# Kernel tuning notes

Measured on AMD Instinct MI355X. Metric: run time of the kernel, lower is better.

Reference implementation:

```python
import jax, jax.numpy as jnp
import numpy as np

N_NODES = 50000


def _gcn_conv(x, row, col, W, b, n_nodes):
    """PyG GCNConv: symmetric-normalized scatter-add aggregation.
    row/col already include self-loops. x: [N, Fin], W: [Fin, Fout]."""
    h = x @ W  # [N, Fout]
    deg = jax.ops.segment_sum(jnp.ones(col.shape[0], x.dtype), col,
                              num_segments=n_nodes)  # in-degree incl. self-loops
    dis = jnp.where(deg > 0, jax.lax.rsqrt(deg), 0.0)  # deg^{-1/2}
    norm = dis[row] * dis[col]  # [E+N]
    msg = h[row] * norm[:, None]  # gather + scale, [E+N, Fout]
    out = jax.ops.segment_sum(msg, col, num_segments=n_nodes)  # scatter-add
    return out + b


def setup_inputs() -> dict:
    key = jax.random.key(0)
    k1, k2, k3, k4 = jax.random.split(key, 4)
    N, E, FIN, FH = N_NODES, 800000, 512, 512
    x = jax.random.normal(k1, (N, FIN), dtype=jnp.float32)
    edge_index = jax.random.randint(k2, (2, E), 0, N, dtype=jnp.int64)
    W1 = jax.random.normal(k3, (FIN, FH), dtype=jnp.float32) * (1.0 / np.sqrt(FIN))
    b1 = jnp.zeros((FH,), jnp.float32)
    W2 = jax.random.normal(k4, (FH, FH), dtype=jnp.float32) * (1.0 / np.sqrt(FH))
    b2 = jnp.zeros((FH,), jnp.float32)
    return {"x": x, "edge_index": edge_index, "W1": W1, "b1": b1,
            "W2": W2, "b2": b2}


def reference(x, edge_index, W1, b1, W2, b2):
    n = x.shape[0]
    loops = jnp.arange(n, dtype=edge_index.dtype)
    row = jnp.concatenate([edge_index[0], loops])  # sources
    col = jnp.concatenate([edge_index[1], loops])  # targets
    h = _gcn_conv(x, row, col, W1, b1, n)
    h = jax.nn.relu(h)
    return _gcn_conv(h, row, col, W2, b2, n)
```

## Files before the change

kernel.cpp:

```cpp
#include <hip/hip_runtime.h>
#include <hip/hip_bf16.h>

typedef short short8 __attribute__((ext_vector_type(8)));
typedef unsigned short u16x8 __attribute__((ext_vector_type(8)));
typedef float f32x4 __attribute__((ext_vector_type(4)));

#define AS1 __attribute__((address_space(1)))
#define AS3 __attribute__((address_space(3)))

__device__ __forceinline__ void gload16(const void* g, void* l) {
  __builtin_amdgcn_global_load_lds((AS1 void*)g, (AS3 void*)l, 16, 0, 0);
}

__device__ __forceinline__ unsigned short f2bf(float f) {
  unsigned u = __float_as_uint(f);
  u = (u + 0x7FFF + ((u >> 16) & 1)) >> 16;
  return (unsigned short)u;
}
__device__ __forceinline__ float bf2f(unsigned short u) {
  return __uint_as_float(((unsigned)u) << 16);
}

__global__ void prep_kernel(const float4* __restrict__ x4, ushort4* __restrict__ xb4, int n4,
                            const float* __restrict__ W1, unsigned short* __restrict__ W1t,
                            const float* __restrict__ W2, unsigned short* __restrict__ W2t) {
  const int nthr = gridDim.x * 256;
  for (int i = blockIdx.x * 256 + threadIdx.x; i < n4; i += nthr) {
    float4 v = x4[i];
    ushort4 o;
    o.x = f2bf(v.x); o.y = f2bf(v.y); o.z = f2bf(v.z); o.w = f2bf(v.w);
    xb4[i] = o;
  }
  for (int idx = blockIdx.x * 256 + threadIdx.x; idx < 512 * 512; idx += nthr) {
    const int k = idx >> 9, n = idx & 511;
    W1t[n * 512 + k] = f2bf(W1[idx]);
    W2t[n * 512 + k] = f2bf(W2[idx]);
  }
}

__global__ void detect64_kernel(const int* __restrict__ ei32, int* __restrict__ flag) {
  if (blockIdx.x == 0 && threadIdx.x == 0) {
    int f = 1;
    for (int i = 0; i < 64; ++i)
      if (ei32[2 * i + 1] != 0) { f = 0; break; }
    *flag = f;
  }
}

__global__ void count_kernel(const int* __restrict__ ei32, const int* __restrict__ flag,
                             int* __restrict__ cnt, int E) {
  int e = blockIdx.x * 256 + threadIdx.x;
  if (e >= E) return;
  int c = (*flag) ? ei32[2 * E + 2 * e] : ei32[E + e];
  atomicAdd(&cnt[c], 1);
}

__global__ void __launch_bounds__(1024) scan_bsum_kernel(const int* __restrict__ cnt,
                                                         int* __restrict__ bsum, int n) {
  __shared__ int ws[16];
  const int tid = threadIdx.x, lane = tid & 63, wid = tid >> 6;
  const int i = blockIdx.x * 1024 + tid;
  int x = (i < n) ? cnt[i] : 0;
#pragma unroll
  for (int d = 1; d < 64; d <<= 1) x += __shfl_xor(x, d, 64);
  if (lane == 0) ws[wid] = x;
  __syncthreads();
  if (tid == 0) {
    int s = 0;
#pragma unroll
    for (int w = 0; w < 16; ++w) s += ws[w];
    bsum[blockIdx.x] = s;
  }
}

__global__ void scan_boff_kernel(int* __restrict__ bsum, int* __restrict__ total, int B) {
  const int lane = threadIdx.x;
  const int v = (lane < B) ? bsum[lane] : 0;
  int x = v;
#pragma unroll
  for (int d = 1; d < 64; d <<= 1) {
    int y = __shfl_up(x, d, 64);
    if (lane >= d) x += y;
  }
  if (lane < B) bsum[lane] = x - v;
  if (lane == B - 1) *total = x;
}

__global__ void __launch_bounds__(1024) scan_fill_kernel(const int* __restrict__ cnt,
    const int* __restrict__ boff, int* __restrict__ ptr, int* __restrict__ cur,
    float* __restrict__ dis, int n) {
  __shared__ int ws[16];
  const int tid = threadIdx.x, lane = tid & 63, wid = tid >> 6;
  const int i = blockIdx.x * 1024 + tid;
  const int v = (i < n) ? cnt[i] : 0;
  int x = v;
#pragma unroll
  for (int d = 1; d < 64; d <<= 1) {
    int y = __shfl_up(x, d, 64);
    if (lane >= d) x += y;
  }
  if (lane == 63) ws[wid] = x;
  __syncthreads();
  if (tid < 16) {
    int wv = ws[tid];
    int wx = wv;
#pragma unroll
    for (int d = 1; d < 16; d <<= 1) {
      int y = __shfl_up(wx, d, 64);
      if (tid >= d) wx += y;
    }
    ws[tid] = wx - wv;
  }
  __syncthreads();
  if (i < n) {
    const int excl = boff[blockIdx.x] + ws[wid] + (x - v);
    ptr[i] = excl;
    cur[i] = excl;
    dis[i] = rsqrtf((float)(v + 1));
  }
}

__global__ void fill_kernel(const int* __restrict__ ei32, const int* __restrict__ flag,
                            int* __restrict__ cur, int* __restrict__ eidx, int E) {
  int e = blockIdx.x * 256 + threadIdx.x;
  if (e >= E) return;
  int is64 = *flag;
  int r = is64 ? ei32[2 * e] : ei32[e];
  int c = is64 ? ei32[2 * E + 2 * e] : ei32[E + e];
  int pos = atomicAdd(&cur[c], 1);
  eidx[pos] = r;
}

__global__ void __launch_bounds__(256) gemm_kernel(const unsigned short* __restrict__ A,
                                                   const unsigned short* __restrict__ Bt,
                                                   const float* __restrict__ dscale,
                                                   unsigned short* __restrict__ C, int M) {
  __shared__ alignas(128) unsigned short As[2][8192];
  __shared__ alignas(128) unsigned short Bs[2][8192];
  const int tid = threadIdx.x;
  const int wave = tid >> 6, lane = tid & 63;
  const int wm = wave >> 1, wn = wave & 1;

  const int nbm = (M + 127) >> 7;
  const int nwg = nbm * 4;
  const int orig = blockIdx.x;
  const int xcd = orig & 7;
  const int q8 = nwg >> 3, r8 = nwg & 7;
  const int wg = (xcd < r8 ? xcd * (q8 + 1) : r8 * (q8 + 1) + (xcd - r8) * q8) + (orig >> 3);
  const int bn = wg & 3;
  const int bm = wg >> 2;

  const int lr = lane >> 3, ls = lane & 7;
  const int fr = lane & 15, ks = lane >> 4;

  f32x4 acc[4][4] = {};

#define STAGE(BUF, KO)                                                                     \
  {                                                                                        \
    _Pragma("unroll") for (int i = 0; i < 4; ++i) {                                        \
      int ra = bm * 128 + i * 32 + wave * 8 + lr;                                          \
      ra = ra < M ? ra : M - 1;                                                            \
      gload16(A + (size_t)ra * 512 + (KO) + ((ls ^ (lr & 7)) << 3),                        \
              &As[BUF][(i * 32 + wave * 8) * 64]);                                         \
      const int rb = bn * 128 + i * 32 + wave * 8 + lr;                                    \
      gload16(Bt + (size_t)rb * 512 + (KO) + ((ls ^ (lr & 7)) << 3),                       \
              &Bs[BUF][(i * 32 + wave * 8) * 64]);                                         \
    }                                                                                      \
  }

  STAGE(0, 0)
  __syncthreads();

  int buf = 0;
  for (int kt = 0; kt < 8; ++kt) {
    if (kt < 7) STAGE(buf ^ 1, (kt + 1) * 64)

    short8 af[2][4], bfg[2][4];
#pragma unroll
    for (int m = 0; m < 4; ++m) {
      const int tr = wm * 64 + m * 16 + fr;
      af[0][m] = *(const short8*)&As[buf][tr * 64 + (((ks * 8)      ) ^ ((tr & 7) << 3))];
      af[1][m] = *(const short8*)&As[buf][tr * 64 + (((ks * 8) + 32 ) ^ ((tr & 7) << 3))];
    }
#pragma unroll
    for (int n = 0; n < 4; ++n) {
      const int tb = wn * 64 + n * 16 + fr;
      bfg[0][n] = *(const short8*)&Bs[buf][tb * 64 + (((ks * 8)      ) ^ ((tb & 7) << 3))];
      bfg[1][n] = *(const short8*)&Bs[buf][tb * 64 + (((ks * 8) + 32 ) ^ ((tb & 7) << 3))];
    }
#pragma unroll
    for (int kk = 0; kk < 2; ++kk)
#pragma unroll
      for (int m = 0; m < 4; ++m)
#pragma unroll
        for (int n = 0; n < 4; ++n)
          acc[m][n] = __builtin_amdgcn_mfma_f32_16x16x32_bf16(af[kk][m], bfg[kk][n], acc[m][n], 0, 0, 0);

    __syncthreads();
    buf ^= 1;
  }
#undef STAGE

  const int rbase = bm * 128 + wm * 64 + (lane >> 4) * 4;
  const int cbase = bn * 128 + wn * 64 + (lane & 15);
#pragma unroll
  for (int m = 0; m < 4; ++m)
#pragma unroll
    for (int j = 0; j < 4; ++j) {
      const int r = rbase + m * 16 + j;
      if (r < M) {
        const float ds = dscale[r];
#pragma unroll
        for (int n = 0; n < 4; ++n)
          C[(size_t)r * 512 + cbase + n * 16] = f2bf(acc[m][n][j] * ds);
      }
    }
}

template <bool FINAL>
__global__ void __launch_bounds__(256) agg_kernel(const unsigned short* __restrict__ h,
    const int* __restrict__ eidx, const int* __restrict__ ptr, const float* __restrict__ dis,
    const float* __restrict__ bias, void* __restrict__ outv, int n) {
  const int tid = threadIdx.x;
  const int lane = tid & 63;
  const int slice = blockIdx.x & 7;
  const int g = lane >> 3;
  const int c = lane & 7;
  const int node = (int)(blockIdx.x >> 3) * 32 + (tid >> 6) * 8 + g;
  if (node >= n) return;
  const int fbase = slice * 64 + c * 8;

  const int start = ptr[node], end = ptr[node + 1];
  float acc[8] = {0, 0, 0, 0, 0, 0, 0, 0};

  int e = start;
  for (; e + 2 <= end; e += 2) {
    const int s0 = eidx[e], s1 = eidx[e + 1];
    const u16x8 v0 = *(const u16x8*)(h + (size_t)(unsigned)s0 * 512 + fbase);
    const u16x8 v1 = *(const u16x8*)(h + (size_t)(unsigned)s1 * 512 + fbase);
#pragma unroll
    for (int j = 0; j < 8; ++j) acc[j] += bf2f(v0[j]) + bf2f(v1[j]);
  }
  if (e < end) {
    const int s0 = eidx[e];
    const u16x8 v = *(const u16x8*)(h + (size_t)(unsigned)s0 * 512 + fbase);
#pragma unroll
    for (int j = 0; j < 8; ++j) acc[j] += bf2f(v[j]);
  }

  {
    const u16x8 v = *(const u16x8*)(h + (size_t)node * 512 + fbase);
#pragma unroll
    for (int j = 0; j < 8; ++j) acc[j] += bf2f(v[j]);
  }

  const float di = dis[node];
  float b[8];
  *(float4*)&b[0] = *(const float4*)(bias + fbase);
  *(float4*)&b[4] = *(const float4*)(bias + fbase + 4);

  if (FINAL) {
    float* out = (float*)outv;
    float4 o0, o1;
    o0.x = acc[0] * di + b[0]; o0.y = acc[1] * di + b[1];
    o0.z = acc[2] * di + b[2]; o0.w = acc[3] * di + b[3];
    o1.x = acc[4] * di + b[4]; o1.y = acc[5] * di + b[5];
    o1.z = acc[6] * di + b[6]; o1.w = acc[7] * di + b[7];
    *(float4*)(out + (size_t)node * 512 + fbase) = o0;
    *(float4*)(out + (size_t)node * 512 + fbase + 4) = o1;
  } else {
    unsigned short* out = (unsigned short*)outv;
    u16x8 o;
#pragma unroll
    for (int j = 0; j < 8; ++j) {
      const float t = acc[j] * di + b[j];
      o[j] = f2bf(t > 0.0f ? t : 0.0f);
    }
    *(u16x8*)(out + (size_t)node * 512 + fbase) = o;
  }
}

extern "C" void kernel_launch(void* const* d_in, const int* in_sizes, int n_in,
                              void* d_out, int out_size, void* d_ws, size_t ws_size,
                              hipStream_t stream) {
  const float* x  = (const float*)d_in[0];
  const int*   ei = (const int*)d_in[1];
  const float* W1 = (const float*)d_in[2];
  const float* b1 = (const float*)d_in[3];
  const float* W2 = (const float*)d_in[4];
  const float* b2 = (const float*)d_in[5];
  float* out = (float*)d_out;

  const int M = in_sizes[0] / 512;
  const int E = in_sizes[1] / 2;

  auto alignup = [](size_t v) { return (v + 255) & ~(size_t)255; };
  char* p = (char*)d_ws;
  unsigned short* xb  = (unsigned short*)p; p += alignup((size_t)M * 512 * 2);
  unsigned short* h1b = (unsigned short*)p; p += alignup((size_t)M * 512 * 2);
  unsigned short* r1b = (unsigned short*)p; p += alignup((size_t)M * 512 * 2);
  unsigned short* w1b = (unsigned short*)p; p += alignup(512 * 512 * 2);
  unsigned short* w2b = (unsigned short*)p; p += alignup(512 * 512 * 2);
  float* dis = (float*)p; p += alignup((size_t)M * 4);
  int* ptr   = (int*)p;   p += alignup((size_t)(M + 1) * 4);
  int* cur   = (int*)p;   p += alignup((size_t)M * 4);
  int* eidx  = (int*)p;   p += alignup((size_t)E * 4);
  int* flag  = (int*)p;   p += alignup(256);
  int* bsum  = (int*)p;   p += alignup(1024);
  int* cnt = (int*)h1b;
  unsigned short* h2b = xb;

  hipMemsetAsync(cnt, 0, (size_t)M * 4, stream);
  detect64_kernel<<<1, 64, 0, stream>>>(ei, flag);

  prep_kernel<<<2048, 256, 0, stream>>>((const float4*)x, (ushort4*)xb, M * 128,
                                        W1, w1b, W2, w2b);

  const int B = (M + 1023) / 1024;
  count_kernel<<<(E + 255) / 256, 256, 0, stream>>>(ei, flag, cnt, E);
  scan_bsum_kernel<<<B, 1024, 0, stream>>>(cnt, bsum, M);
  scan_boff_kernel<<<1, 64, 0, stream>>>(bsum, ptr + M, B);
  scan_fill_kernel<<<B, 1024, 0, stream>>>(cnt, bsum, ptr, cur, dis, M);
  fill_kernel<<<(E + 255) / 256, 256, 0, stream>>>(ei, flag, cur, eidx, E);

  const int nwg = ((M + 127) / 128) * 4;
  const int nag = ((M + 31) / 32) * 8;
  gemm_kernel<<<nwg, 256, 0, stream>>>(xb, w1b, dis, h1b, M);
  agg_kernel<false><<<nag, 256, 0, stream>>>(h1b, eidx, ptr, dis, b1, (void*)r1b, M);
  gemm_kernel<<<nwg, 256, 0, stream>>>(r1b, w2b, dis, h2b, M);
  agg_kernel<true><<<nag, 256, 0, stream>>>(h2b, eidx, ptr, dis, b2, (void*)out, M);
}
```

Baseline: 427.1 us.

## Store hidden features in column-slice-major layout for gather locality

The GEMM outputs and the layer-1 aggregation output are now stored as eight 64-column slices, each contiguous across all nodes, instead of row-major 512-wide rows. Each aggregation block handles one slice, so its random neighbor gathers hit a 6.4 MB region rather than the whole feature matrix, which should improve L2/MALL reuse. The second GEMM reads its A operand from this sliced layout. The cost is more scattered 2-byte epilogue stores in the GEMM and a different A-tile address pattern.

```diff
diff --git a/kernel.cpp b/kernel.cpp
--- a/kernel.cpp
+++ b/kernel.cpp
@@ -131,6 +131,7 @@
   eidx[pos] = r;
 }
 
+template <bool BA, bool BC>
 __global__ void __launch_bounds__(256) gemm_kernel(const unsigned short* __restrict__ A,
                                                    const unsigned short* __restrict__ Bt,
                                                    const float* __restrict__ dscale,
@@ -160,8 +161,9 @@
     _Pragma("unroll") for (int i = 0; i < 4; ++i) {                                        \
       int ra = bm * 128 + i * 32 + wave * 8 + lr;                                          \
       ra = ra < M ? ra : M - 1;                                                            \
-      gload16(A + (size_t)ra * 512 + (KO) + ((ls ^ (lr & 7)) << 3),                        \
-              &As[BUF][(i * 32 + wave * 8) * 64]);                                         \
+      const size_t aoff = BA ? ((size_t)(KO)*M + (size_t)ra * 64 + ((ls ^ (lr & 7)) << 3)) \
+                             : ((size_t)ra * 512 + (KO) + ((ls ^ (lr & 7)) << 3));         \
+      gload16(A + aoff, &As[BUF][(i * 32 + wave * 8) * 64]);                               \
       const int rb = bn * 128 + i * 32 + wave * 8 + lr;                                    \
       gload16(Bt + (size_t)rb * 512 + (KO) + ((ls ^ (lr & 7)) << 3),                       \
               &Bs[BUF][(i * 32 + wave * 8) * 64]);                                         \
@@ -203,6 +205,7 @@
 
   const int rbase = bm * 128 + wm * 64 + (lane >> 4) * 4;
   const int cbase = bn * 128 + wn * 64 + (lane & 15);
+  const size_t hseg = (size_t)M * 64;
 #pragma unroll
   for (int m = 0; m < 4; ++m)
 #pragma unroll
@@ -211,8 +214,15 @@
       if (r < M) {
         const float ds = dscale[r];
 #pragma unroll
-        for (int n = 0; n < 4; ++n)
-          C[(size_t)r * 512 + cbase + n * 16] = f2bf(acc[m][n][j] * ds);
+        for (int n = 0; n < 4; ++n) {
+          const unsigned short val = f2bf(acc[m][n][j] * ds);
+          if (BC) {
+            const int col = cbase + n * 16;
+            C[(size_t)(col >> 6) * hseg + (size_t)r * 64 + (col & 63)] = val;
+          } else {
+            C[(size_t)r * 512 + cbase + n * 16] = val;
+          }
+        }
       }
     }
 }
@@ -228,7 +238,9 @@
   const int c = lane & 7;
   const int node = (int)(blockIdx.x >> 3) * 32 + (tid >> 6) * 8 + g;
   if (node >= n) return;
-  const int fbase = slice * 64 + c * 8;
+
+  const unsigned short* hs = h + (size_t)slice * ((size_t)n * 64);
+  const int coff = c * 8;
 
   const int start = ptr[node], end = ptr[node + 1];
   float acc[8] = {0, 0, 0, 0, 0, 0, 0, 0};
@@ -236,28 +248,29 @@
   int e = start;
   for (; e + 2 <= end; e += 2) {
     const int s0 = eidx[e], s1 = eidx[e + 1];
-    const u16x8 v0 = *(const u16x8*)(h + (size_t)(unsigned)s0 * 512 + fbase);
-    const u16x8 v1 = *(const u16x8*)(h + (size_t)(unsigned)s1 * 512 + fbase);
+    const u16x8 v0 = *(const u16x8*)(hs + (size_t)(unsigned)s0 * 64 + coff);
+    const u16x8 v1 = *(const u16x8*)(hs + (size_t)(unsigned)s1 * 64 + coff);
 #pragma unroll
     for (int j = 0; j < 8; ++j) acc[j] += bf2f(v0[j]) + bf2f(v1[j]);
   }
   if (e < end) {
     const int s0 = eidx[e];
-    const u16x8 v = *(const u16x8*)(h + (size_t)(unsigned)s0 * 512 + fbase);
+    const u16x8 v = *(const u16x8*)(hs + (size_t)(unsigned)s0 * 64 + coff);
 #pragma unroll
     for (int j = 0; j < 8; ++j) acc[j] += bf2f(v[j]);
   }
 
   {
-    const u16x8 v = *(const u16x8*)(h + (size_t)node * 512 + fbase);
+    const u16x8 v = *(const u16x8*)(hs + (size_t)node * 64 + coff);
 #pragma unroll
     for (int j = 0; j < 8; ++j) acc[j] += bf2f(v[j]);
   }
 
   const float di = dis[node];
+  const int fcol = slice * 64 + coff;
   float b[8];
-  *(float4*)&b[0] = *(const float4*)(bias + fbase);
-  *(float4*)&b[4] = *(const float4*)(bias + fbase + 4);
+  *(float4*)&b[0] = *(const float4*)(bias + fcol);
+  *(float4*)&b[4] = *(const float4*)(bias + fcol + 4);
 
   if (FINAL) {
     float* out = (float*)outv;
@@ -266,8 +279,8 @@
     o0.z = acc[2] * di + b[2]; o0.w = acc[3] * di + b[3];
     o1.x = acc[4] * di + b[4]; o1.y = acc[5] * di + b[5];
     o1.z = acc[6] * di + b[6]; o1.w = acc[7] * di + b[7];
-    *(float4*)(out + (size_t)node * 512 + fbase) = o0;
-    *(float4*)(out + (size_t)node * 512 + fbase + 4) = o1;
+    *(float4*)(out + (size_t)node * 512 + fcol) = o0;
+    *(float4*)(out + (size_t)node * 512 + fcol + 4) = o1;
   } else {
     unsigned short* out = (unsigned short*)outv;
     u16x8 o;
@@ -276,7 +289,7 @@
       const float t = acc[j] * di + b[j];
       o[j] = f2bf(t > 0.0f ? t : 0.0f);
     }
-    *(u16x8*)(out + (size_t)node * 512 + fbase) = o;
+    *(u16x8*)(out + (size_t)slice * ((size_t)n * 64) + (size_t)node * 64 + coff) = o;
   }
 }
 
@@ -325,8 +338,8 @@
 
   const int nwg = ((M + 127) / 128) * 4;
   const int nag = ((M + 31) / 32) * 8;
-  gemm_kernel<<<nwg, 256, 0, stream>>>(xb, w1b, dis, h1b, M);
+  gemm_kernel<false, true><<<nwg, 256, 0, stream>>>(xb, w1b, dis, h1b, M);
   agg_kernel<false><<<nag, 256, 0, stream>>>(h1b, eidx, ptr, dis, b1, (void*)r1b, M);
-  gemm_kernel<<<nwg, 256, 0, stream>>>(r1b, w2b, dis, h2b, M);
+  gemm_kernel<true, true><<<nwg, 256, 0, stream>>>(r1b, w2b, dis, h2b, M);
   agg_kernel<true><<<nag, 256, 0, stream>>>(h2b, eidx, ptr, dis, b2, (void*)out, M);
 }
```

Measured after the change: 410.9 us. -3.8%, faster.
